# Performance work log

Hardware: AMD Instinct MI355X
Metric: run time of the kernel (lower is better)

The kernel has to match this reference:

```python
import jax, jax.numpy as jnp
import numpy as np

CORR = 5          # corr_size (patch_size)
UP = 2            # upsample_param
CH = [512, 1024, 512, 256, 256, 256]
SZ = [64, 32, 16, 8, 4, 2]   # pyramid spatial sizes; UP*2**i upsamples all to 128
B = 2
P = CORR * CORR

def upsample_nearest(x, f):
    # nn.Upsample(scale_factor=f, mode='nearest') for integer f
    return jnp.repeat(jnp.repeat(x, f, axis=2), f, axis=3)

def correlate(f1, f2):
    # spatial_correlation_sample: kernel=1, patch=CORR, stride=1, padding=0, dilation_patch=1
    # out[b, pi*CORR+pj, y, x] = sum_c f1[b,c,y,x] * f2[b,c,y+pi-r,x+pj-r] (zeros out of range)
    r = CORR // 2
    b, c, h, w = f1.shape
    f2p = jnp.pad(f2, ((0, 0), (0, 0), (r, r), (r, r)))
    outs = []
    for pi in range(CORR):
        for pj in range(CORR):
            sh = jax.lax.dynamic_slice(f2p, (0, 0, pi, pj), (b, c, h, w))
            outs.append(jnp.sum(f1 * sh, axis=1))
    return jnp.stack(outs, axis=1)  # [B, P, h, w]

def avgpool(x):
    # AvgPool2d(kernel_size=3, stride=2, padding=1), count_include_pad=True (torch default)
    s = jax.lax.reduce_window(x, 0.0, jax.lax.add, (1, 1, 3, 3), (1, 1, 2, 2), ((0, 0), (0, 0), (1, 1), (1, 1)))
    return s / 9.0

def conv3x3(x, w, b):
    y = jax.lax.conv_general_dilated(x, w, (1, 1), ((1, 1), (1, 1)), dimension_numbers=("NCHW", "OIHW", "NCHW"))
    return y + b[None, :, None, None]

def level_step(feat1, feat2, h_pre, c_pre, w, b, lvl):
    f = UP * (2 ** lvl)
    u1 = upsample_nearest(feat1, f)
    u2 = upsample_nearest(feat2, f)
    corr = jax.nn.leaky_relu(correlate(u1, u2), 0.01)
    # int(log2(up_W / feat_W)) pools; this is <= 6 so only avg_pooling1 is ever used
    for _ in range(int(np.log2(u1.shape[3] // feat1.shape[3]))):
        corr = avgpool(corr)
    gates = conv3x3(jnp.concatenate([corr, h_pre], axis=1), w, b)
    i = jax.nn.sigmoid(gates[:, :P])
    fg = jax.nn.sigmoid(gates[:, P:2 * P])
    o = jax.nn.sigmoid(gates[:, 2 * P:3 * P])
    g = jnp.tanh(gates[:, 3 * P:])
    c_next = fg * c_pre + i * g
    h_next = o * jnp.tanh(c_next)
    return h_next, c_next

def setup_inputs():
    keys = jax.random.split(jax.random.key(0), 40)
    d = {}
    k = 0
    for i in range(6):
        d[f"x{i}"] = jax.random.normal(keys[k], (B, CH[i], SZ[i], SZ[i]), jnp.float32); k += 1
        d[f"xp{i}"] = jax.random.normal(keys[k], (B, CH[i], SZ[i], SZ[i]), jnp.float32); k += 1
        d[f"h{i}"] = jax.random.normal(keys[k], (B, P, SZ[i], SZ[i]), jnp.float32); k += 1
        d[f"c{i}"] = jax.random.normal(keys[k], (B, P, SZ[i], SZ[i]), jnp.float32); k += 1
    for i in range(6):
        d[f"W{i}"] = jax.random.normal(keys[k], (4 * P, 2 * P, 3, 3), jnp.float32) * 0.05; k += 1
        d[f"b{i}"] = jnp.zeros((4 * P,), jnp.float32)
    return d

def reference(x0, x1, x2, x3, x4, x5, xp0, xp1, xp2, xp3, xp4, xp5,
              h0, h1, h2, h3, h4, h5, c0, c1, c2, c3, c4, c5,
              W0, W1, W2, W3, W4, W5, b0, b1, b2, b3, b4, b5):
    xs = [x0, x1, x2, x3, x4, x5]
    xps = [xp0, xp1, xp2, xp3, xp4, xp5]
    hs = [h0, h1, h2, h3, h4, h5]
    cs = [c0, c1, c2, c3, c4, c5]
    Ws = [W0, W1, W2, W3, W4, W5]
    bs = [b0, b1, b2, b3, b4, b5]
    outs = []
    for lvl in range(6):
        h_next, c_next = level_step(xs[lvl], xps[lvl], hs[lvl], cs[lvl], Ws[lvl], bs[lvl], lvl)
        outs.extend([h_next, c_next])
    return tuple(outs)
```

## Files before the change

kernel.cpp:

```cpp
#include <hip/hip_runtime.h>

#define NB 2
#define PP 25
#define NLVL 6

struct Params {
  const float* x1[NLVL];
  const float* x2[NLVL];
  const float* h[NLVL];
  const float* c[NLVL];
  const float* W[NLVL];
  const float* bias[NLVL];
  float* Dpart[NLVL];
  float* D[NLVL];
  float* pooled[NLVL];
  float* WT[NLVL];
  float* gates[NLVL];
  float* hout[NLVL];
  float* cout[NLVL];
};

__device__ __forceinline__ float lrelu(float v) { return v > 0.f ? v : 0.01f * v; }

__global__ __launch_bounds__(256) void repack_kernel(Params pr) {
  const int lvl = blockIdx.y;
  const float* W = pr.W[lvl];
  float* WT = pr.WT[lvl];
  for (int i = blockIdx.x * 256 + threadIdx.x; i < 100 * 450; i += gridDim.x * 256) {
    const int oc = i / 450;
    const int r = i - oc * 450;
    WT[r * 100 + oc] = W[i];
  }
}

__global__ __launch_bounds__(256) void dcorr_kernel(Params pr) {
  static const int SZt[6] = {64, 32, 16, 8, 4, 2};
  static const int CHt[6] = {512, 1024, 512, 256, 256, 256};
  static const int NCH[6] = {16, 16, 4, 1, 1, 1};
  static const int LGQ[6] = {4, 3, 2, 0, 0, 0};
  const int lvl = blockIdx.y;
  const int S = SZt[lvl], C = CHt[lvl], nch = NCH[lvl];
  const int rows = NB * S;
  const int bid = blockIdx.x;
  if (bid >= rows * nch) return;
  const int row = bid / nch;
  const int chunk = bid - row * nch;
  const int b = row / S, yb = row - b * S;
  const int tid = threadIdx.x;
  const size_t nlev = (size_t)NB * S * S * 9;
  float* part = pr.Dpart[lvl] + (size_t)chunk * nlev;

  __shared__ float red[9216];

  if (S >= 16) {
    const int lgq = LGQ[lvl];
    const int xqn = S >> 2;
    const int cgn = 256 >> lgq;
    const int xq = tid & (xqn - 1);
    const int cg = tid >> lgq;
    const int chpc = C / nch;
    const int cpt = chpc / cgn;
    const int xb0 = xq << 2;

    const float* f1b = pr.x1[lvl] + (size_t)b * C * S * S + (size_t)yb * S + xb0;
    const float* f2b = pr.x2[lvl] + (size_t)b * C * S * S;

    float acc[9][4];
#pragma unroll
    for (int jj = 0; jj < 9; ++jj)
#pragma unroll
      for (int j = 0; j < 4; ++j) acc[jj][j] = 0.f;

    const int c0 = chunk * chpc + cg;
    for (int t = 0; t < cpt; ++t) {
      const int cc = c0 + t * cgn;
      const float4 f1 = *(const float4*)(f1b + (size_t)cc * S * S);
      const float f1a[4] = {f1.x, f1.y, f1.z, f1.w};
      const float* p2 = f2b + (size_t)cc * S * S;
#pragma unroll
      for (int dy = 0; dy < 3; ++dy) {
        const int yy = yb + dy - 1;
        if (yy < 0 || yy >= S) continue;
        const float* prow = p2 + (size_t)yy * S;
        const float4 m = *(const float4*)(prow + xb0);
        const float lm = (xb0 > 0) ? prow[xb0 - 1] : 0.f;
        const float rm = (xb0 + 4 < S) ? prow[xb0 + 4] : 0.f;
        const float wl[4] = {lm, m.x, m.y, m.z};
        const float wc[4] = {m.x, m.y, m.z, m.w};
        const float wr[4] = {m.y, m.z, m.w, rm};
#pragma unroll
        for (int j = 0; j < 4; ++j) {
          acc[dy * 3 + 0][j] = fmaf(f1a[j], wl[j], acc[dy * 3 + 0][j]);
          acc[dy * 3 + 1][j] = fmaf(f1a[j], wc[j], acc[dy * 3 + 1][j]);
          acc[dy * 3 + 2][j] = fmaf(f1a[j], wr[j], acc[dy * 3 + 2][j]);
        }
      }
    }

    const int n = S * 9;
#pragma unroll
    for (int jj = 0; jj < 9; ++jj)
#pragma unroll
      for (int j = 0; j < 4; ++j)
        red[cg * n + (xb0 + j) * 9 + jj] = acc[jj][j];
    __syncthreads();
    for (int g = cgn >> 1; g >= 1; g >>= 1) {
      for (int i = tid; i < g * n; i += 256) {
        const int c = i / n, e = i - c * n;
        red[c * n + e] += red[(c + g) * n + e];
      }
      __syncthreads();
    }
    float* out = part + (size_t)(b * S + yb) * S * 9;
    for (int i = tid; i < n; i += 256) out[i] = red[i];
  } else {
    const int lg = (S == 8) ? 3 : ((S == 4) ? 2 : 1);
    const int xb = tid & (S - 1), cg = tid >> lg;
    const int NG = 256 >> lg;
    const int cpt = C / NG;

    const float* f1base = pr.x1[lvl] + (size_t)b * C * S * S + (size_t)yb * S + xb;
    const float* f2base = pr.x2[lvl] + (size_t)b * C * S * S;

    float acc[9];
#pragma unroll
    for (int j = 0; j < 9; ++j) acc[j] = 0.f;

    for (int t = 0; t < cpt; ++t) {
      const int cc = cg + t * NG;
      const float f1 = f1base[(size_t)cc * S * S];
      const float* p2 = f2base + (size_t)cc * S * S;
#pragma unroll
      for (int dy = 0; dy < 3; ++dy) {
        const int yy = yb + dy - 1;
        if (yy < 0 || yy >= S) continue;
        const float* prow = p2 + yy * S;
#pragma unroll
        for (int dx = 0; dx < 3; ++dx) {
          const int xx = xb + dx - 1;
          const float v = (xx >= 0 && xx < S) ? prow[xx] : 0.f;
          acc[dy * 3 + dx] += f1 * v;
        }
      }
    }

#pragma unroll
    for (int j = 0; j < 9; ++j) red[tid * 9 + j] = acc[j];
    __syncthreads();
    for (int g = NG >> 1; g >= 1; g >>= 1) {
      if (cg < g) {
#pragma unroll
        for (int j = 0; j < 9; ++j) red[tid * 9 + j] += red[(tid + g * S) * 9 + j];
      }
      __syncthreads();
    }
    if (cg == 0) {
      float* Dp = part + ((size_t)(b * S + yb) * S + xb) * 9;
#pragma unroll
      for (int j = 0; j < 9; ++j) Dp[j] = red[tid * 9 + j];
    }
  }
}

__global__ __launch_bounds__(256) void dreduce_kernel(Params pr) {
  static const int SZt[6] = {64, 32, 16, 8, 4, 2};
  static const int NCH[6] = {16, 16, 4, 1, 1, 1};
  const int lvl = blockIdx.y;
  const int S = SZt[lvl], nch = NCH[lvl];
  const int n = NB * S * S * 9;
  const int i = blockIdx.x * 256 + threadIdx.x;
  if (i >= n) return;
  const float* part = pr.Dpart[lvl];
  float s = 0.f;
  for (int c = 0; c < nch; ++c) s += part[(size_t)c * n + i];
  pr.D[lvl][i] = lrelu(s);
}

__global__ __launch_bounds__(256) void pool_kernel(Params pr) {
  static const int SZt[6] = {64, 32, 16, 8, 4, 2};
  static const int NYC[6] = {8, 4, 2, 1, 1, 1};
  static const int LGS[6] = {6, 5, 4, 3, 2, 1};
  const int lvl = blockIdx.y;
  const int S = SZt[lvl], k = lvl + 1, f = 1 << k, nyc = NYC[lvl], lgS = LGS[lvl];
  const int nyo = S / nyc;
  const int bid = blockIdx.x;
  if (bid >= 50 * nyc) return;
  const int yc = bid / 50;
  const int bp = bid - yc * 50;
  const int b = bp / 25, p = bp - (bp / 25) * 25;
  const int dpy = p / 5 - 2, dpx = p - (p / 5) * 5 - 2;
  const int tid = threadIdx.x;
  const int yo0 = yc * nyo;

  __shared__ float ckb[2][130], clb[2][66];
  __shared__ float Dl[5184];
  __shared__ float tmp[1024];

  if (tid == 0) { ckb[0][0] = 1.f; clb[0][0] = 1.f; }
  __syncthreads();
  int rj = 0, cur = 0;
  for (int j = 0; j < k; ++j) {
    const int half = 1 << j, rn = 2 * half - 1;
    float cknew = 0.f, clnew = 0.f;
    if (tid <= 2 * rn) {
      const int t = tid - rn;
#pragma unroll
      for (int e = -1; e <= 1; ++e) {
        const int u = t + e * half;
        if (u >= -rj && u <= rj) cknew += ckb[cur][u + rj];
      }
      cknew *= (1.f / 3.f);
    }
    if (tid < 2 * half) {
      const int y = tid;
      float s = (y < half) ? clb[cur][y] : 0.f;
      const int u = y - half;
      if (u >= -rj && u <= rj) s += ckb[cur][u + rj];
      clnew = s * (1.f / 3.f);
    }
    __syncthreads();
    if (tid <= 2 * rn) ckb[cur ^ 1][tid] = cknew;
    if (tid < 2 * half) clb[cur ^ 1][tid] = clnew;
    __syncthreads();
    cur ^= 1;
    rj = rn;
  }
  const float* ck = ckb[cur];
  const float* cl = clb[cur];

  const int yb0 = (yo0 > 0) ? yo0 - 1 : 0;
  const int nyb = (yo0 + nyo - 1) - yb0 + 1;
  const float* Dg = pr.D[lvl] + (size_t)b * S * S * 9 + (size_t)yb0 * S * 9;
  const int nload = nyb * S * 9;
  for (int i = tid; i < nload; i += 256) Dl[i] = Dg[i];
  __syncthreads();

  for (int item = tid; item < nyo * 128; item += 256) {
    const int yol = item >> 7, x = item & 127;
    const int yo = yo0 + yol;
    const int xb = x >> k, tx = x & (f - 1);
    const int txp = tx + dpx;
    const int dxi = (txp < 0) ? 0 : ((txp >= f) ? 2 : 1);
    float sum = 0.f;
    if (yo == 0) {
      for (int y = 0; y < f; ++y) {
        const int typ = y + dpy;
        const int dyi = (typ < 0) ? 0 : ((typ >= f) ? 2 : 1);
        sum += cl[y] * Dl[((0 - yb0) * S + xb) * 9 + dyi * 3 + dxi];
      }
    } else {
      const int ylo = yo * f - (f - 1);
      for (int t = 0; t < 2 * f - 1; ++t) {
        const int y = ylo + t;
        const int yb = y >> k, ty = y & (f - 1);
        const int typ = ty + dpy;
        const int dyi = (typ < 0) ? 0 : ((typ >= f) ? 2 : 1);
        sum += ck[t] * Dl[((yb - yb0) * S + xb) * 9 + dyi * 3 + dxi];
      }
    }
    tmp[yol * 128 + x] = sum;
  }
  __syncthreads();

  float* out = pr.pooled[lvl] + (size_t)(b * PP + p) * S * S;
  for (int item = tid; item < nyo * S; item += 256) {
    const int yol = item >> lgS, xo = item & (S - 1);
    float sum = 0.f;
    if (xo == 0) {
      for (int x = 0; x < f; ++x) sum += cl[x] * tmp[yol * 128 + x];
    } else {
      const int xlo = xo * f - (f - 1);
      for (int t = 0; t < 2 * f - 1; ++t) sum += ck[t] * tmp[yol * 128 + xlo + t];
    }
    out[(size_t)(yo0 + yol) * S + xo] = sum;
  }
}

__global__ __launch_bounds__(128) void conv_kernel(Params pr) {
  static const int SZt[6] = {64, 32, 16, 8, 4, 2};
  static const int XT[6]  = {32, 32, 16, 8, 4, 2};
  static const int WD[6]  = {36, 36, 20, 12, 8, 8};
  const int lvl = blockIdx.y;
  const int S = SZt[lvl], xtile = XT[lvl], width = WD[lvl];
  const int ntx = S / xtile;
  const int nblk = NB * S * ntx;
  const int bid = blockIdx.x;
  if (bid >= nblk) return;
  const int b = bid / (S * ntx);
  const int rem = bid - b * (S * ntx);
  const int y = rem / ntx;
  const int xt = rem - y * ntx;
  const int x0 = xt * xtile;
  const int q = blockIdx.z;
  const int tid = threadIdx.x;

  __shared__ float in_lds[3 * 50 * 36 + 8];
  const float* pooled = pr.pooled[lvl] + (size_t)b * PP * S * S;
  const float* hin = pr.h[lvl] + (size_t)b * PP * S * S;
  {
    int i = tid;
    int r = i / width;
    int j = i - r * width;
    while (r < 150) {
      const int ky = r / 50;
      const int ic = r - ky * 50;
      const int yy = y + ky - 1;
      const int x = x0 + j - 1;
      float v = 0.f;
      if (yy >= 0 && yy < S && x >= 0 && x < S)
        v = (ic < PP) ? pooled[((size_t)ic * S + yy) * S + x]
                      : hin[((size_t)(ic - PP) * S + yy) * S + x];
      in_lds[r * width + j] = v;
      j += 128;
      while (j >= width) { j -= width; ++r; }
    }
  }
  __syncthreads();

  const int XC = (xtile >= 8) ? 8 : xtile;
  const int nxc = xtile / XC;
  const int nitems = PP * nxc;
  if (tid >= nitems) return;
  const int xs = tid / 25;
  const int p = tid - xs * 25;
  const int oc = q * PP + p;
  const float* wp = pr.WT[lvl] + oc;

  float w[9], wn[9];
#pragma unroll
  for (int t = 0; t < 9; ++t) w[t] = wp[t * 100];

  float acc[8];
#pragma unroll
  for (int xx = 0; xx < 8; ++xx) acc[xx] = 0.f;

  const int xoff = xs * XC;
  for (int ic = 0; ic < 50; ++ic) {
    if (ic < 49) {
      const float* wq = wp + (size_t)(ic + 1) * 900;
#pragma unroll
      for (int t = 0; t < 9; ++t) wn[t] = wq[t * 100];
    }
#pragma unroll
    for (int ky = 0; ky < 3; ++ky) {
      const float* row = &in_lds[(ky * 50 + ic) * width + xoff];
      const float4 A = ((const float4*)row)[0];
      const float4 Bv = ((const float4*)row)[1];
      const float4 Cv = ((const float4*)row)[2];
      const float sg[12] = {A.x, A.y, A.z, A.w, Bv.x, Bv.y, Bv.z, Bv.w,
                            Cv.x, Cv.y, Cv.z, Cv.w};
      const float w0 = w[ky * 3], w1 = w[ky * 3 + 1], w2 = w[ky * 3 + 2];
#pragma unroll
      for (int xx = 0; xx < 8; ++xx)
        acc[xx] = fmaf(w0, sg[xx], fmaf(w1, sg[xx + 1], fmaf(w2, sg[xx + 2], acc[xx])));
    }
#pragma unroll
    for (int t = 0; t < 9; ++t) w[t] = wn[t];
  }

  const float bb = pr.bias[lvl][oc];
  float* g = pr.gates[lvl] + ((size_t)(q * NB + b) * PP + p) * S * S +
             (size_t)y * S + x0 + xoff;
  if (XC == 8) {
    ((float4*)g)[0] = make_float4(acc[0] + bb, acc[1] + bb, acc[2] + bb, acc[3] + bb);
    ((float4*)g)[1] = make_float4(acc[4] + bb, acc[5] + bb, acc[6] + bb, acc[7] + bb);
  } else if (XC == 4) {
    ((float4*)g)[0] = make_float4(acc[0] + bb, acc[1] + bb, acc[2] + bb, acc[3] + bb);
  } else {
    g[0] = acc[0] + bb;
    g[1] = acc[1] + bb;
  }
}

__global__ __launch_bounds__(256) void lstm_kernel(Params pr) {
  static const int SZt[6] = {64, 32, 16, 8, 4, 2};
  const int lvl = blockIdx.y;
  const int S = SZt[lvl];
  const int n4 = (NB * PP * S * S) >> 2;
  const int i4 = blockIdx.x * 256 + threadIdx.x;
  if (i4 >= n4) return;
  const float4* g0 = (const float4*)pr.gates[lvl];
  const float4 vi = g0[i4];
  const float4 vf = g0[n4 + i4];
  const float4 vo = g0[2 * n4 + i4];
  const float4 vg = g0[3 * n4 + i4];
  const float4 vc = ((const float4*)pr.c[lvl])[i4];
  float4 hn, cn;
  const float* gi = (const float*)&vi;
  const float* gf = (const float*)&vf;
  const float* go = (const float*)&vo;
  const float* gg = (const float*)&vg;
  const float* cp = (const float*)&vc;
  float* hp = (float*)&hn;
  float* cq = (float*)&cn;
#pragma unroll
  for (int j = 0; j < 4; ++j) {
    const float i_ = 1.f / (1.f + __expf(-gi[j]));
    const float f_ = 1.f / (1.f + __expf(-gf[j]));
    const float o_ = 1.f / (1.f + __expf(-go[j]));
    const float g_ = 1.f - 2.f / (__expf(2.f * gg[j]) + 1.f);
    const float c_ = f_ * cp[j] + i_ * g_;
    const float t2 = 1.f - 2.f / (__expf(2.f * c_) + 1.f);
    cq[j] = c_;
    hp[j] = o_ * t2;
  }
  ((float4*)pr.hout[lvl])[i4] = hn;
  ((float4*)pr.cout[lvl])[i4] = cn;
}

extern "C" void kernel_launch(void* const* d_in, const int* in_sizes, int n_in,
                              void* d_out, int out_size, void* d_ws, size_t ws_size,
                              hipStream_t stream) {
  static const int SZ[NLVL] = {64, 32, 16, 8, 4, 2};
  static const int NCH[NLVL] = {16, 16, 4, 1, 1, 1};

  Params pr;
  float* ws = (float*)d_ws;
  size_t off = 0;
  for (int l = 0; l < NLVL; ++l) {
    pr.Dpart[l] = ws + off;
    off += (size_t)NCH[l] * NB * SZ[l] * SZ[l] * 9;
  }
  for (int l = 0; l < NLVL; ++l) { pr.D[l] = ws + off; off += (size_t)NB * SZ[l] * SZ[l] * 9; }
  for (int l = 0; l < NLVL; ++l) { pr.pooled[l] = ws + off; off += (size_t)NB * PP * SZ[l] * SZ[l]; }
  for (int l = 0; l < NLVL; ++l) { pr.WT[l] = ws + off; off += 100 * 450; }
  for (int l = 0; l < NLVL; ++l) { pr.gates[l] = ws + off; off += (size_t)4 * NB * PP * SZ[l] * SZ[l]; }

  float* out = (float*)d_out;
  size_t ooff = 0;
  for (int l = 0; l < NLVL; ++l) {
    pr.hout[l] = out + ooff; ooff += (size_t)NB * PP * SZ[l] * SZ[l];
    pr.cout[l] = out + ooff; ooff += (size_t)NB * PP * SZ[l] * SZ[l];
  }

  for (int l = 0; l < NLVL; ++l) {
    pr.x1[l] = (const float*)d_in[4 * l + 0];
    pr.x2[l] = (const float*)d_in[4 * l + 1];
    pr.h[l]  = (const float*)d_in[4 * l + 2];
    pr.c[l]  = (const float*)d_in[4 * l + 3];
    pr.W[l]    = (const float*)d_in[24 + 2 * l];
    pr.bias[l] = (const float*)d_in[25 + 2 * l];
  }

  repack_kernel<<<dim3(45, NLVL), 256, 0, stream>>>(pr);
  dcorr_kernel<<<dim3(2048, NLVL), 256, 0, stream>>>(pr);
  dreduce_kernel<<<dim3(288, NLVL), 256, 0, stream>>>(pr);
  pool_kernel<<<dim3(400, NLVL), 256, 0, stream>>>(pr);
  conv_kernel<<<dim3(256, NLVL, 4), 128, 0, stream>>>(pr);
  lstm_kernel<<<dim3(200, NLVL), 256, 0, stream>>>(pr);
}
```

Before: 269.2 us.

## Fuse conv with LSTM gates for large levels and split small levels

For the three large pyramid levels, a new conv kernel computes all 100 gate channels per block, reading inputs straight from global memory through a four-deep register prefetch pipeline instead of staging them in LDS. It then applies the LSTM cell in-block from an LDS gate buffer, so the gates tensor is never written to or read back from global memory for these levels. Small levels keep an LDS-based conv and a separate LSTM kernel with fewer launched blocks. The fused path raises register pressure and repeats input loads across the 100 output-channel threads, relying on cache hits.

```diff
diff --git a/kernel.cpp b/kernel.cpp
--- a/kernel.cpp
+++ b/kernel.cpp
@@ -276,53 +276,169 @@
   }
 }
 
-__global__ __launch_bounds__(128) void conv_kernel(Params pr) {
-  static const int SZt[6] = {64, 32, 16, 8, 4, 2};
-  static const int XT[6]  = {32, 32, 16, 8, 4, 2};
-  static const int WD[6]  = {36, 36, 20, 12, 8, 8};
+struct WB { float w[9]; };
+struct IB { float4 a[3]; float4 b2[3]; float l[3]; float r[3]; };
+
+__device__ __forceinline__ void loadW(WB& wb, const float* wp, int ic) {
+#pragma unroll
+  for (int t = 0; t < 9; ++t) wb.w[t] = wp[(ic * 9 + t) * 100];
+}
+
+__device__ __forceinline__ void loadI(IB& ib, const float* pb, const float* hb,
+                                      int ic, int SS, int S, int y, int x0) {
+  const float* cb = (ic < PP) ? (pb + (size_t)ic * SS) : (hb + (size_t)(ic - PP) * SS);
+#pragma unroll
+  for (int dy = 0; dy < 3; ++dy) {
+    const int yy = y + dy - 1;
+    const bool yok = (yy >= 0) && (yy < S);
+    const float* rb = cb + yy * S;
+    if (yok) {
+      ib.a[dy] = *(const float4*)(rb + x0);
+      ib.b2[dy] = *(const float4*)(rb + x0 + 4);
+      ib.l[dy] = (x0 > 0) ? rb[x0 - 1] : 0.f;
+      ib.r[dy] = (x0 + 8 < S) ? rb[x0 + 8] : 0.f;
+    } else {
+      ib.a[dy] = make_float4(0.f, 0.f, 0.f, 0.f);
+      ib.b2[dy] = make_float4(0.f, 0.f, 0.f, 0.f);
+      ib.l[dy] = 0.f;
+      ib.r[dy] = 0.f;
+    }
+  }
+}
+
+__device__ __forceinline__ void fmab(float acc[8], const WB& wb, const IB& ib) {
+#pragma unroll
+  for (int dy = 0; dy < 3; ++dy) {
+    const float sg[10] = {ib.l[dy],  ib.a[dy].x,  ib.a[dy].y,  ib.a[dy].z,
+                          ib.a[dy].w, ib.b2[dy].x, ib.b2[dy].y, ib.b2[dy].z,
+                          ib.b2[dy].w, ib.r[dy]};
+    const float w0 = wb.w[dy * 3], w1 = wb.w[dy * 3 + 1], w2 = wb.w[dy * 3 + 2];
+#pragma unroll
+    for (int xx = 0; xx < 8; ++xx)
+      acc[xx] = fmaf(w0, sg[xx], fmaf(w1, sg[xx + 1], fmaf(w2, sg[xx + 2], acc[xx])));
+  }
+}
+
+__global__ __launch_bounds__(256) void conv_big_kernel(Params pr) {
+  static const int SZt[3] = {64, 32, 16};
   const int lvl = blockIdx.y;
-  const int S = SZt[lvl], xtile = XT[lvl], width = WD[lvl];
-  const int ntx = S / xtile;
-  const int nblk = NB * S * ntx;
+  const int S = SZt[lvl];
+  const int SS = S * S;
+  const int nxt = S >> 4;
+  const int nblk = NB * S * nxt;
   const int bid = blockIdx.x;
   if (bid >= nblk) return;
-  const int b = bid / (S * ntx);
-  const int rem = bid - b * (S * ntx);
-  const int y = rem / ntx;
-  const int xt = rem - y * ntx;
-  const int x0 = xt * xtile;
+  const int b = bid / (S * nxt);
+  const int rem = bid - b * (S * nxt);
+  const int y = rem / nxt;
+  const int xt = rem - y * nxt;
+  const int tid = threadIdx.x;
+  const int xs = tid >> 7;
+  const int r = tid & 127;
+  const int x0 = xt * 16 + xs * 8;
+
+  __shared__ float glds[100 * 16];
+
+  const float* pb = pr.pooled[lvl] + (size_t)b * PP * SS;
+  const float* hb = pr.h[lvl] + (size_t)b * PP * SS;
+
+  if (r < 100) {
+    const int oc = r;
+    const float* wp = pr.WT[lvl] + oc;
+
+    WB w0b, w1b, w2b, w3b;
+    IB i0b, i1b, i2b, i3b;
+    loadW(w0b, wp, 0); loadI(i0b, pb, hb, 0, SS, S, y, x0);
+    loadW(w1b, wp, 1); loadI(i1b, pb, hb, 1, SS, S, y, x0);
+    loadW(w2b, wp, 2); loadI(i2b, pb, hb, 2, SS, S, y, x0);
+    loadW(w3b, wp, 3); loadI(i3b, pb, hb, 3, SS, S, y, x0);
+
+    float acc[8];
+#pragma unroll
+    for (int xx = 0; xx < 8; ++xx) acc[xx] = 0.f;
+
+    for (int ic = 0; ic < 44; ic += 4) {
+      fmab(acc, w0b, i0b); loadW(w0b, wp, ic + 4); loadI(i0b, pb, hb, ic + 4, SS, S, y, x0);
+      fmab(acc, w1b, i1b); loadW(w1b, wp, ic + 5); loadI(i1b, pb, hb, ic + 5, SS, S, y, x0);
+      fmab(acc, w2b, i2b); loadW(w2b, wp, ic + 6); loadI(i2b, pb, hb, ic + 6, SS, S, y, x0);
+      fmab(acc, w3b, i3b); loadW(w3b, wp, ic + 7); loadI(i3b, pb, hb, ic + 7, SS, S, y, x0);
+    }
+    fmab(acc, w0b, i0b); loadW(w0b, wp, 48); loadI(i0b, pb, hb, 48, SS, S, y, x0);
+    fmab(acc, w1b, i1b); loadW(w1b, wp, 49); loadI(i1b, pb, hb, 49, SS, S, y, x0);
+    fmab(acc, w2b, i2b);
+    fmab(acc, w3b, i3b);
+    fmab(acc, w0b, i0b);
+    fmab(acc, w1b, i1b);
+
+    const float bb = pr.bias[lvl][oc];
+#pragma unroll
+    for (int xx = 0; xx < 8; ++xx) glds[oc * 16 + xs * 8 + xx] = acc[xx] + bb;
+  }
+  __syncthreads();
+
+  if (tid < 50) {
+    const int xs2 = tid / 25;
+    const int p = tid - xs2 * 25;
+    const int xoff = xs2 * 8;
+    const size_t base = ((size_t)(b * PP + p) * S + y) * S + xt * 16 + xoff;
+    const float4 c0 = *(const float4*)(pr.c[lvl] + base);
+    const float4 c1 = *(const float4*)(pr.c[lvl] + base + 4);
+    const float cp[8] = {c0.x, c0.y, c0.z, c0.w, c1.x, c1.y, c1.z, c1.w};
+    float hn[8], cn[8];
+#pragma unroll
+    for (int j = 0; j < 8; ++j) {
+      const float gi = glds[(0 * PP + p) * 16 + xoff + j];
+      const float gf = glds[(1 * PP + p) * 16 + xoff + j];
+      const float go = glds[(2 * PP + p) * 16 + xoff + j];
+      const float gg = glds[(3 * PP + p) * 16 + xoff + j];
+      const float i_ = 1.f / (1.f + __expf(-gi));
+      const float f_ = 1.f / (1.f + __expf(-gf));
+      const float o_ = 1.f / (1.f + __expf(-go));
+      const float g_ = 1.f - 2.f / (__expf(2.f * gg) + 1.f);
+      const float c_ = f_ * cp[j] + i_ * g_;
+      const float t2 = 1.f - 2.f / (__expf(2.f * c_) + 1.f);
+      cn[j] = c_;
+      hn[j] = o_ * t2;
+    }
+    *(float4*)(pr.hout[lvl] + base) = make_float4(hn[0], hn[1], hn[2], hn[3]);
+    *(float4*)(pr.hout[lvl] + base + 4) = make_float4(hn[4], hn[5], hn[6], hn[7]);
+    *(float4*)(pr.cout[lvl] + base) = make_float4(cn[0], cn[1], cn[2], cn[3]);
+    *(float4*)(pr.cout[lvl] + base + 4) = make_float4(cn[4], cn[5], cn[6], cn[7]);
+  }
+}
+
+__global__ __launch_bounds__(128) void conv_small_kernel(Params pr) {
+  static const int SZt[6] = {64, 32, 16, 8, 4, 2};
+  static const int WD[6]  = {36, 36, 20, 12, 8, 8};
+  const int lvl = blockIdx.y + 3;
+  const int S = SZt[lvl], width = WD[lvl];
+  const int nblk = NB * S;
+  const int bid = blockIdx.x;
+  if (bid >= nblk) return;
+  const int b = bid / S;
+  const int y = bid - b * S;
   const int q = blockIdx.z;
   const int tid = threadIdx.x;
 
-  __shared__ float in_lds[3 * 50 * 36 + 8];
+  __shared__ float in_lds[3 * 50 * 12 + 8];
   const float* pooled = pr.pooled[lvl] + (size_t)b * PP * S * S;
   const float* hin = pr.h[lvl] + (size_t)b * PP * S * S;
-  {
-    int i = tid;
-    int r = i / width;
-    int j = i - r * width;
-    while (r < 150) {
-      const int ky = r / 50;
-      const int ic = r - ky * 50;
-      const int yy = y + ky - 1;
-      const int x = x0 + j - 1;
-      float v = 0.f;
-      if (yy >= 0 && yy < S && x >= 0 && x < S)
-        v = (ic < PP) ? pooled[((size_t)ic * S + yy) * S + x]
-                      : hin[((size_t)(ic - PP) * S + yy) * S + x];
-      in_lds[r * width + j] = v;
-      j += 128;
-      while (j >= width) { j -= width; ++r; }
-    }
+  for (int i = tid; i < 150 * width; i += 128) {
+    const int rr = i / width, j = i - rr * width;
+    const int ky = rr / 50;
+    const int ic = rr - ky * 50;
+    const int yy = y + ky - 1;
+    const int x = j - 1;
+    float v = 0.f;
+    if (yy >= 0 && yy < S && x >= 0 && x < S)
+      v = (ic < PP) ? pooled[((size_t)ic * S + yy) * S + x]
+                    : hin[((size_t)(ic - PP) * S + yy) * S + x];
+    in_lds[rr * width + j] = v;
   }
   __syncthreads();
 
-  const int XC = (xtile >= 8) ? 8 : xtile;
-  const int nxc = xtile / XC;
-  const int nitems = PP * nxc;
-  if (tid >= nitems) return;
-  const int xs = tid / 25;
-  const int p = tid - xs * 25;
+  if (tid >= PP) return;
+  const int p = tid;
   const int oc = q * PP + p;
   const float* wp = pr.WT[lvl] + oc;
 
@@ -334,7 +450,6 @@
 #pragma unroll
   for (int xx = 0; xx < 8; ++xx) acc[xx] = 0.f;
 
-  const int xoff = xs * XC;
   for (int ic = 0; ic < 50; ++ic) {
     if (ic < 49) {
       const float* wq = wp + (size_t)(ic + 1) * 900;
@@ -343,38 +458,27 @@
     }
 #pragma unroll
     for (int ky = 0; ky < 3; ++ky) {
-      const float* row = &in_lds[(ky * 50 + ic) * width + xoff];
-      const float4 A = ((const float4*)row)[0];
-      const float4 Bv = ((const float4*)row)[1];
-      const float4 Cv = ((const float4*)row)[2];
-      const float sg[12] = {A.x, A.y, A.z, A.w, Bv.x, Bv.y, Bv.z, Bv.w,
-                            Cv.x, Cv.y, Cv.z, Cv.w};
+      const float* row = &in_lds[(ky * 50 + ic) * width];
       const float w0 = w[ky * 3], w1 = w[ky * 3 + 1], w2 = w[ky * 3 + 2];
 #pragma unroll
       for (int xx = 0; xx < 8; ++xx)
-        acc[xx] = fmaf(w0, sg[xx], fmaf(w1, sg[xx + 1], fmaf(w2, sg[xx + 2], acc[xx])));
+        if (xx < S)
+          acc[xx] = fmaf(w0, row[xx], fmaf(w1, row[xx + 1], fmaf(w2, row[xx + 2], acc[xx])));
     }
 #pragma unroll
     for (int t = 0; t < 9; ++t) w[t] = wn[t];
   }
 
   const float bb = pr.bias[lvl][oc];
-  float* g = pr.gates[lvl] + ((size_t)(q * NB + b) * PP + p) * S * S +
-             (size_t)y * S + x0 + xoff;
-  if (XC == 8) {
-    ((float4*)g)[0] = make_float4(acc[0] + bb, acc[1] + bb, acc[2] + bb, acc[3] + bb);
-    ((float4*)g)[1] = make_float4(acc[4] + bb, acc[5] + bb, acc[6] + bb, acc[7] + bb);
-  } else if (XC == 4) {
-    ((float4*)g)[0] = make_float4(acc[0] + bb, acc[1] + bb, acc[2] + bb, acc[3] + bb);
-  } else {
-    g[0] = acc[0] + bb;
-    g[1] = acc[1] + bb;
-  }
-}
-
-__global__ __launch_bounds__(256) void lstm_kernel(Params pr) {
+  float* g = pr.gates[lvl] + ((size_t)(q * NB + b) * PP + p) * S * S + (size_t)y * S;
+#pragma unroll
+  for (int xx = 0; xx < 8; ++xx)
+    if (xx < S) g[xx] = acc[xx] + bb;
+}
+
+__global__ __launch_bounds__(256) void lstm_small_kernel(Params pr) {
   static const int SZt[6] = {64, 32, 16, 8, 4, 2};
-  const int lvl = blockIdx.y;
+  const int lvl = blockIdx.y + 3;
   const int S = SZt[lvl];
   const int n4 = (NB * PP * S * S) >> 2;
   const int i4 = blockIdx.x * 256 + threadIdx.x;
@@ -446,6 +550,7 @@
   dcorr_kernel<<<dim3(2048, NLVL), 256, 0, stream>>>(pr);
   dreduce_kernel<<<dim3(288, NLVL), 256, 0, stream>>>(pr);
   pool_kernel<<<dim3(400, NLVL), 256, 0, stream>>>(pr);
-  conv_kernel<<<dim3(256, NLVL, 4), 128, 0, stream>>>(pr);
-  lstm_kernel<<<dim3(200, NLVL), 256, 0, stream>>>(pr);
-}
+  conv_big_kernel<<<dim3(512, 3), 256, 0, stream>>>(pr);
+  conv_small_kernel<<<dim3(16, 3, 4), 128, 0, stream>>>(pr);
+  lstm_small_kernel<<<dim3(4, 3), 256, 0, stream>>>(pr);
+}
```

Result: slower. 437.1 us (+62.4%).
